# Kernel tuning notes

Hardware: AMD Instinct MI355X
Metric: run time of the kernel (lower is better)

## Reference

```python
import jax, jax.numpy as jnp
import numpy as np

THRESHOLD = 0.5
MAX_POINTS = 10000
NORMALIZE = True
BIDIRECTIONAL = True
INF = jnp.float32(1e30)


def _voxels_to_points(vox):
    # vox: (D, H, W). Returns padded points (MAX_POINTS, 3) and validity mask.
    D, H, W = vox.shape
    flat = vox.reshape(-1)
    active = flat > THRESHOLD
    n_active = jnp.sum(active.astype(jnp.int32))
    # Stable argsort puts active voxel indices first (deterministic stand-in
    # for torch's randperm subsampling when n_active > MAX_POINTS).
    order = jnp.argsort(jnp.where(active, 0, 1).astype(jnp.int32))
    idx = order[:MAX_POINTS]
    valid = jnp.arange(MAX_POINTS) < jnp.minimum(n_active, MAX_POINTS)
    d = idx // (H * W)
    h = (idx // W) % H
    w = idx % W
    pts = jnp.stack([d, h, w], axis=-1).astype(jnp.float32)  # (MAX_POINTS, 3)
    if NORMALIZE:
        pts = pts / (D - 1) * 2.0 - 1.0
    pts = jnp.where(valid[:, None], pts, 0.0)
    return pts, valid


def _chamfer_single(p1, v1, p2, v2):
    # p1: (N,3), p2: (M,3) padded; v1/v2 are validity masks.
    n1 = jnp.sum(p1 * p1, axis=1)  # (N,)
    n2 = jnp.sum(p2 * p2, axis=1)  # (M,)
    dist = n1[:, None] + n2[None, :] - 2.0 * (p1 @ p2.T)  # (N, M)
    dist = jnp.maximum(dist, 0.0)
    c1 = jnp.maximum(jnp.sum(v1.astype(jnp.float32)), 1.0)
    c2 = jnp.maximum(jnp.sum(v2.astype(jnp.float32)), 1.0)
    min_1to2 = jnp.min(jnp.where(v2[None, :], dist, INF), axis=1)  # (N,)
    loss = jnp.sum(jnp.where(v1, min_1to2, 0.0)) / c1
    if BIDIRECTIONAL:
        min_2to1 = jnp.min(jnp.where(v1[:, None], dist, INF), axis=0)  # (M,)
        loss = loss + jnp.sum(jnp.where(v2, min_2to1, 0.0)) / c2
    return loss


def setup_inputs() -> dict:
    key = jax.random.key(0)
    k1, k2 = jax.random.split(key)
    pred = jax.random.uniform(k1, (4, 1, 64, 64, 64), dtype=jnp.float32)
    target = jax.random.uniform(k2, (4, 1, 64, 64, 64), dtype=jnp.float32)
    return {"pred": pred, "target": target}


def reference(pred, target):
    B = pred.shape[0]
    total = jnp.float32(0.0)
    n_valid = jnp.float32(0.0)
    for b in range(B):  # small fixed batch loop (per-sample dist matrix is 10k x 10k)
        p1, v1 = _voxels_to_points(pred[b, 0])
        p2, v2 = _voxels_to_points(target[b, 0])
        has_pts = jnp.logical_and(jnp.any(v1), jnp.any(v2))
        cd = _chamfer_single(p1, v1, p2, v2)
        total = total + jnp.where(has_pts, cd, 0.0)
        n_valid = n_valid + has_pts.astype(jnp.float32)
    return jnp.where(n_valid > 0, total / jnp.maximum(n_valid, 1.0), 0.0)
```

## Files before the change

kernel.cpp:

```cpp
#include <hip/hip_runtime.h>
#include <hip/hip_bf16.h>


#define NVOX      262144
#define NCHUNK    256
#define MAXPTS    10000
#define PTS_PAD   10240
#define NCLOUD    8
#define NTASK     8
#define NRB       40
#define NBM_WORDS 8192
#define SCALE     (2.0f/63.0f)

#define WS_TOTALS   0
#define WS_COUNTS   1024
#define WS_OFFSETS  16384
#define WS_QLIST    32768
#define WS_BITMAP   360448
#define WS_BSUM     622592

__device__ __forceinline__ const float* cloud_src(const float* pred, const float* tgt, int cloud) {
    const float* base = (cloud & 1) ? tgt : pred;
    return base + (size_t)(cloud >> 1) * NVOX;
}

__global__ void k_count(const float* __restrict__ pred, const float* __restrict__ tgt,
                        int* __restrict__ counts, unsigned* __restrict__ bitmap) {
    int gi = blockIdx.x * 256 + threadIdx.x;
    if (gi < NCLOUD * NBM_WORDS) bitmap[gi] = 0u;
    int cloud = blockIdx.x >> 8;
    int chunk = blockIdx.x & 255;
    int t = threadIdx.x;
    const float* src = cloud_src(pred, tgt, cloud) + chunk * 1024;
    float4 v = reinterpret_cast<const float4*>(src)[t];
    int cnt = (v.x > 0.5f) + (v.y > 0.5f) + (v.z > 0.5f) + (v.w > 0.5f);
    __shared__ int s[256];
    s[t] = cnt; __syncthreads();
    for (int o = 128; o > 0; o >>= 1) {
        if (t < o) s[t] += s[t + o];
        __syncthreads();
    }
    if (t == 0) counts[cloud * NCHUNK + chunk] = s[0];
}

__global__ void k_scan(const int* __restrict__ counts, int* __restrict__ offsets,
                       int* __restrict__ totals) {
    int cloud = blockIdx.x;
    int t = threadIdx.x;
    int c = counts[cloud * NCHUNK + t];
    __shared__ int s[256];
    s[t] = c; __syncthreads();
    for (int o = 1; o < 256; o <<= 1) {
        int v = (t >= o) ? s[t - o] : 0;
        __syncthreads();
        s[t] += v;
        __syncthreads();
    }
    offsets[cloud * NCHUNK + t] = s[t] - c;
    if (t == 255) totals[cloud] = s[255];
}

__global__ void k_compact(const float* __restrict__ pred, const float* __restrict__ tgt,
                          const int* __restrict__ offsets,
                          int* __restrict__ qlist, unsigned* __restrict__ bitmap) {
    int cloud = blockIdx.x >> 8;
    int chunk = blockIdx.x & 255;
    int t = threadIdx.x;
    const float* src = cloud_src(pred, tgt, cloud) + chunk * 1024;
    float4 v = reinterpret_cast<const float4*>(src)[t];
    int f0 = v.x > 0.5f, f1 = v.y > 0.5f, f2 = v.z > 0.5f, f3 = v.w > 0.5f;
    int cnt = f0 + f1 + f2 + f3;
    __shared__ int s[256];
    s[t] = cnt; __syncthreads();
    for (int o = 1; o < 256; o <<= 1) {
        int x = (t >= o) ? s[t - o] : 0;
        __syncthreads();
        s[t] += x;
        __syncthreads();
    }
    int rank = offsets[cloud * NCHUNK + chunk] + (s[t] - cnt);
    int eidx = chunk * 1024 + t * 4;
    int flags[4] = {f0, f1, f2, f3};
    #pragma unroll
    for (int e = 0; e < 4; ++e) {
        if (flags[e]) {
            if (rank < MAXPTS) {
                int idx = eidx + e;
                qlist[cloud * PTS_PAD + rank] = idx;
                atomicOr(&bitmap[cloud * NBM_WORDS + (idx >> 5)], 1u << (idx & 31));
            }
            rank++;
        }
    }
}

__global__ __launch_bounds__(256) void k_nn(const int* __restrict__ qlist,
                                            const unsigned* __restrict__ bitmap,
                                            const int* __restrict__ totals,
                                            float* __restrict__ bsum) {
    int task = blockIdx.x / NRB;
    int blk  = blockIdx.x % NRB;
    int b = task >> 1, dir = task & 1;
    int qc = 2 * b + dir;
    int rc = 2 * b + (dir ^ 1);
    int tid = threadIdx.x;

    __shared__ unsigned bm[NBM_WORDS];
    {
        const uint4* src = (const uint4*)(bitmap + rc * NBM_WORDS);
        uint4* dst = (uint4*)bm;
        #pragma unroll
        for (int i = 0; i < 8; ++i) dst[tid + i * 256] = src[tid + i * 256];
    }
    __syncthreads();

    int countQ = min(totals[qc], MAXPTS);
    int countR = min(totals[rc], MAXPTS);
    int qi = blk * 256 + tid;

    float contrib = 0.f;
    if (qi < countQ && countR > 0) {
        int idx = qlist[qc * PTS_PAD + qi];
        int qd = idx >> 12, qh = (idx >> 6) & 63, qw = idx & 63;
        int best = 0x7fffffff;
        for (int r = 0; r <= 63; ++r) {
            if (r * r > best) break;
            for (int dz = -r; dz <= r; ++dz) {
                int z = qd + dz;
                if ((unsigned)z > 63u) continue;
                int zb = z << 12;
                int dz2 = dz * dz;
                for (int dy = -r; dy <= r; ++dy) {
                    int y = qh + dy;
                    if ((unsigned)y > 63u) continue;
                    int zyb = zb | (y << 6);
                    int dzy2 = dz2 + dy * dy;
                    bool face = (dz == -r) | (dz == r) | (dy == -r) | (dy == r);
                    if (face) {
                        for (int dx = -r; dx <= r; ++dx) {
                            int w = qw + dx;
                            if ((unsigned)w > 63u) continue;
                            int vid = zyb | w;
                            if ((bm[vid >> 5] >> (vid & 31)) & 1u)
                                best = min(best, dzy2 + dx * dx);
                        }
                    } else {
                        int w0 = qw - r, w1 = qw + r;
                        if ((unsigned)w0 <= 63u) {
                            int vid = zyb | w0;
                            if ((bm[vid >> 5] >> (vid & 31)) & 1u)
                                best = min(best, dzy2 + r * r);
                        }
                        if ((unsigned)w1 <= 63u) {
                            int vid = zyb | w1;
                            if ((bm[vid >> 5] >> (vid & 31)) & 1u)
                                best = min(best, dzy2 + r * r);
                        }
                    }
                }
            }
        }
        const float SC2 = SCALE * SCALE;
        contrib = (float)best * SC2;
    }

    __shared__ float sb[256];
    sb[tid] = contrib; __syncthreads();
    for (int o = 128; o > 0; o >>= 1) {
        if (tid < o) sb[tid] += sb[tid + o];
        __syncthreads();
    }
    if (tid == 0) bsum[task * NRB + blk] = sb[0];
}

__global__ void k_final(const float* __restrict__ bsum, const int* __restrict__ totals,
                        float* __restrict__ out) {
    int t = threadIdx.x;
    __shared__ float sh[NTASK];
    if (t < NTASK) {
        float s = 0.f;
        #pragma unroll
        for (int i = 0; i < NRB; ++i) s += bsum[t * NRB + i];
        sh[t] = s;
    }
    __syncthreads();
    if (t == 0) {
        float total = 0.f, nv = 0.f;
        for (int b = 0; b < 4; ++b) {
            int c1 = min(totals[2 * b], MAXPTS);
            int c2 = min(totals[2 * b + 1], MAXPTS);
            float cd = sh[2 * b] / fmaxf((float)c1, 1.f) + sh[2 * b + 1] / fmaxf((float)c2, 1.f);
            if (c1 > 0 && c2 > 0) { total += cd; nv += 1.f; }
        }
        out[0] = (nv > 0.f) ? total / nv : 0.f;
    }
}

extern "C" void kernel_launch(void* const* d_in, const int* in_sizes, int n_in,
                              void* d_out, int out_size, void* d_ws, size_t ws_size,
                              hipStream_t stream) {
    const float* pred = (const float*)d_in[0];
    const float* tgt  = (const float*)d_in[1];
    float* out = (float*)d_out;

    char* ws = (char*)d_ws;
    int*      totals  = (int*)(ws + WS_TOTALS);
    int*      counts  = (int*)(ws + WS_COUNTS);
    int*      offsets = (int*)(ws + WS_OFFSETS);
    int*      qlist   = (int*)(ws + WS_QLIST);
    unsigned* bitmap  = (unsigned*)(ws + WS_BITMAP);
    float*    bsum    = (float*)(ws + WS_BSUM);

    k_count  <<<NCLOUD * NCHUNK, 256, 0, stream>>>(pred, tgt, counts, bitmap);
    k_scan   <<<NCLOUD,          256, 0, stream>>>(counts, offsets, totals);
    k_compact<<<NCLOUD * NCHUNK, 256, 0, stream>>>(pred, tgt, offsets, qlist, bitmap);
    k_nn     <<<NTASK * NRB,     256, 0, stream>>>(qlist, bitmap, totals, bsum);
    k_final  <<<1, 64, 0, stream>>>(bsum, totals, out);
}
```

Baseline: 58.88 us.

## Fold chunk scan into compaction and add unrolled 3x3x3 fast path for NN search

Removes the separate scan kernel: each compaction block redundantly scans the 256 per-chunk counts in shared memory to get its base offset, and block 0 writes the cloud total. This drops one launch and its dependency gap at the cost of extra per-block scan work. In the nearest-neighbour kernel, the r=0 and r=1 shells are replaced by a fully unrolled 27-voxel check, and the general shell loop from r=2 runs only when nothing was found. With about half the voxels active, the fast path should almost always hit, which reduces branchy loop overhead.

```diff
diff --git a/kernel.cpp b/kernel.cpp
--- a/kernel.cpp
+++ b/kernel.cpp
@@ -14,7 +14,6 @@
 
 #define WS_TOTALS   0
 #define WS_COUNTS   1024
-#define WS_OFFSETS  16384
 #define WS_QLIST    32768
 #define WS_BITMAP   360448
 #define WS_BSUM     622592
@@ -43,29 +42,26 @@
     if (t == 0) counts[cloud * NCHUNK + chunk] = s[0];
 }
 
-__global__ void k_scan(const int* __restrict__ counts, int* __restrict__ offsets,
-                       int* __restrict__ totals) {
-    int cloud = blockIdx.x;
-    int t = threadIdx.x;
-    int c = counts[cloud * NCHUNK + t];
-    __shared__ int s[256];
-    s[t] = c; __syncthreads();
-    for (int o = 1; o < 256; o <<= 1) {
-        int v = (t >= o) ? s[t - o] : 0;
-        __syncthreads();
-        s[t] += v;
-        __syncthreads();
-    }
-    offsets[cloud * NCHUNK + t] = s[t] - c;
-    if (t == 255) totals[cloud] = s[255];
-}
-
 __global__ void k_compact(const float* __restrict__ pred, const float* __restrict__ tgt,
-                          const int* __restrict__ offsets,
+                          const int* __restrict__ counts, int* __restrict__ totals,
                           int* __restrict__ qlist, unsigned* __restrict__ bitmap) {
     int cloud = blockIdx.x >> 8;
     int chunk = blockIdx.x & 255;
     int t = threadIdx.x;
+
+    __shared__ int sc[256];
+    sc[t] = counts[cloud * NCHUNK + t];
+    __syncthreads();
+    for (int o = 1; o < 256; o <<= 1) {
+        int v = (t >= o) ? sc[t - o] : 0;
+        __syncthreads();
+        sc[t] += v;
+        __syncthreads();
+    }
+    if (chunk == 0 && t == 255) totals[cloud] = sc[255];
+    int chunk_base = sc[chunk] - counts[cloud * NCHUNK + chunk];
+    __syncthreads();
+
     const float* src = cloud_src(pred, tgt, cloud) + chunk * 1024;
     float4 v = reinterpret_cast<const float4*>(src)[t];
     int f0 = v.x > 0.5f, f1 = v.y > 0.5f, f2 = v.z > 0.5f, f3 = v.w > 0.5f;
@@ -78,7 +74,7 @@
         s[t] += x;
         __syncthreads();
     }
-    int rank = offsets[cloud * NCHUNK + chunk] + (s[t] - cnt);
+    int rank = chunk_base + (s[t] - cnt);
     int eidx = chunk * 1024 + t * 4;
     int flags[4] = {f0, f1, f2, f3};
     #pragma unroll
@@ -123,45 +119,61 @@
         int idx = qlist[qc * PTS_PAD + qi];
         int qd = idx >> 12, qh = (idx >> 6) & 63, qw = idx & 63;
         int best = 0x7fffffff;
-        for (int r = 0; r <= 63; ++r) {
-            if (r * r > best) break;
-            for (int dz = -r; dz <= r; ++dz) {
-                int z = qd + dz;
-                if ((unsigned)z > 63u) continue;
-                int zb = z << 12;
-                int dz2 = dz * dz;
-                for (int dy = -r; dy <= r; ++dy) {
-                    int y = qh + dy;
-                    if ((unsigned)y > 63u) continue;
-                    int zyb = zb | (y << 6);
-                    int dzy2 = dz2 + dy * dy;
-                    bool face = (dz == -r) | (dz == r) | (dy == -r) | (dy == r);
-                    if (face) {
-                        for (int dx = -r; dx <= r; ++dx) {
-                            int w = qw + dx;
-                            if ((unsigned)w > 63u) continue;
-                            int vid = zyb | w;
-                            if ((bm[vid >> 5] >> (vid & 31)) & 1u)
-                                best = min(best, dzy2 + dx * dx);
-                        }
-                    } else {
-                        int w0 = qw - r, w1 = qw + r;
-                        if ((unsigned)w0 <= 63u) {
-                            int vid = zyb | w0;
-                            if ((bm[vid >> 5] >> (vid & 31)) & 1u)
-                                best = min(best, dzy2 + r * r);
-                        }
-                        if ((unsigned)w1 <= 63u) {
-                            int vid = zyb | w1;
-                            if ((bm[vid >> 5] >> (vid & 31)) & 1u)
-                                best = min(best, dzy2 + r * r);
+
+        #pragma unroll
+        for (int dz = -1; dz <= 1; ++dz)
+        #pragma unroll
+        for (int dy = -1; dy <= 1; ++dy)
+        #pragma unroll
+        for (int dx = -1; dx <= 1; ++dx) {
+            int z = qd + dz, y = qh + dy, w = qw + dx;
+            bool ok = ((unsigned)z < 64u) & ((unsigned)y < 64u) & ((unsigned)w < 64u);
+            int vid = ((z << 12) | (y << 6) | w) & (NVOX - 1);
+            unsigned word = bm[vid >> 5];
+            int d2 = dz * dz + dy * dy + dx * dx;
+            if (ok && ((word >> (vid & 31)) & 1u)) best = min(best, d2);
+        }
+
+        if (best == 0x7fffffff) {
+            for (int r = 2; r <= 63; ++r) {
+                if (r * r > best) break;
+                for (int dz = -r; dz <= r; ++dz) {
+                    int z = qd + dz;
+                    if ((unsigned)z > 63u) continue;
+                    int zb = z << 12;
+                    int dz2 = dz * dz;
+                    for (int dy = -r; dy <= r; ++dy) {
+                        int y = qh + dy;
+                        if ((unsigned)y > 63u) continue;
+                        int zyb = zb | (y << 6);
+                        int dzy2 = dz2 + dy * dy;
+                        bool face = (dz == -r) | (dz == r) | (dy == -r) | (dy == r);
+                        if (face) {
+                            for (int dx = -r; dx <= r; ++dx) {
+                                int w = qw + dx;
+                                if ((unsigned)w > 63u) continue;
+                                int vid = zyb | w;
+                                if ((bm[vid >> 5] >> (vid & 31)) & 1u)
+                                    best = min(best, dzy2 + dx * dx);
+                            }
+                        } else {
+                            int w0 = qw - r, w1 = qw + r;
+                            if ((unsigned)w0 <= 63u) {
+                                int vid = zyb | w0;
+                                if ((bm[vid >> 5] >> (vid & 31)) & 1u)
+                                    best = min(best, dzy2 + r * r);
+                            }
+                            if ((unsigned)w1 <= 63u) {
+                                int vid = zyb | w1;
+                                if ((bm[vid >> 5] >> (vid & 31)) & 1u)
+                                    best = min(best, dzy2 + r * r);
+                            }
                         }
                     }
                 }
             }
         }
-        const float SC2 = SCALE * SCALE;
-        contrib = (float)best * SC2;
+        contrib = (float)best * (SCALE * SCALE);
     }
 
     __shared__ float sb[256];
@@ -206,14 +218,12 @@
     char* ws = (char*)d_ws;
     int*      totals  = (int*)(ws + WS_TOTALS);
     int*      counts  = (int*)(ws + WS_COUNTS);
-    int*      offsets = (int*)(ws + WS_OFFSETS);
     int*      qlist   = (int*)(ws + WS_QLIST);
     unsigned* bitmap  = (unsigned*)(ws + WS_BITMAP);
     float*    bsum    = (float*)(ws + WS_BSUM);
 
     k_count  <<<NCLOUD * NCHUNK, 256, 0, stream>>>(pred, tgt, counts, bitmap);
-    k_scan   <<<NCLOUD,          256, 0, stream>>>(counts, offsets, totals);
-    k_compact<<<NCLOUD * NCHUNK, 256, 0, stream>>>(pred, tgt, offsets, qlist, bitmap);
+    k_compact<<<NCLOUD * NCHUNK, 256, 0, stream>>>(pred, tgt, counts, totals, qlist, bitmap);
     k_nn     <<<NTASK * NRB,     256, 0, stream>>>(qlist, bitmap, totals, bsum);
     k_final  <<<1, 64, 0, stream>>>(bsum, totals, out);
 }
```

Result: faster. 57.37 us (-2.6%).
